# Kernel tuning notes

Measured on AMD Instinct MI355X. Metric: run time of the kernel, lower is better.

Reference implementation:

```python
import jax, jax.numpy as jnp
import numpy as np

NEG = -1000000000.0

def setup_inputs() -> dict:
    key = jax.random.key(0)
    k1, k2, k3, k4 = jax.random.split(key, 4)
    B, S, D = 8, 4096, 256
    query = jax.random.normal(k1, (B, S, D), dtype=jnp.float32)
    k_ = jax.random.normal(k2, (B, S, D), dtype=jnp.float32)
    value = jax.random.normal(k3, (B, S, D), dtype=jnp.float32)
    mask = jax.random.bernoulli(k4, 0.1, (B, S, 1))  # True = masked
    return {"query": query, "key": k_, "value": value, "mask": mask}

def reference(query, key, value, mask):
    # a: [B,S,1] sum of squares of query; b: [B,S,1] for key
    a = jnp.sum(query * query, axis=-1, keepdims=True)
    b = jnp.sum(key * key, axis=-1, keepdims=True)
    # s1 = (K^T / b) @ V  -> [B, D, D]; divide each key row s by b_s
    s1 = jnp.einsum('bsd,bse->bde', key / b, value)
    # score = Q / a, masked rows set to -1e9
    score = query / a
    score = jnp.where(mask, NEG, score)
    s2 = jnp.einsum('bsd,bde->bse', score, s1)
    return s2 / query.shape[-1]
```

## Files before the change

kernel.cpp:

```cpp
#include <hip/hip_runtime.h>

#define BB 8
#define SS 4096
#define DD 256
#define NEGV -1000000000.0f

typedef float f32x4 __attribute__((ext_vector_type(4)));
typedef short s16x8 __attribute__((ext_vector_type(8)));

static __device__ __forceinline__ unsigned short f2bf(float x) {
  unsigned int u = __builtin_bit_cast(unsigned int, x);
  u += 0x7fffu + ((u >> 16) & 1u);
  return (unsigned short)(u >> 16);
}

static __device__ __forceinline__ void gload_lds16(
    const unsigned short* __restrict__ g, unsigned short* l) {
  __builtin_amdgcn_global_load_lds(
      (const __attribute__((address_space(1))) void*)g,
      (__attribute__((address_space(3))) void*)l, 16, 0, 0);
}

__global__ __launch_bounds__(256) void prep_kernel(
    const float* __restrict__ Q, const float* __restrict__ K,
    const float* __restrict__ V, const int* __restrict__ mask,
    unsigned short* __restrict__ QS, unsigned short* __restrict__ KT,
    unsigned short* __restrict__ VT) {
  __shared__ unsigned short tile[64 * 260];
  const int b = blockIdx.y;
  const int s0 = blockIdx.x * 64;
  const int tid = threadIdx.x;
  const int w = tid >> 6, l = tid & 63;

  if (blockIdx.z == 0) {
    float4 reg[16];
    float ps[16];
#pragma unroll
    for (int it = 0; it < 16; ++it) {
      const int row = it * 4 + w;
      reg[it] = *(const float4*)(Q + ((size_t)b * SS + s0 + row) * DD + l * 4);
      ps[it] = reg[it].x * reg[it].x + reg[it].y * reg[it].y +
               reg[it].z * reg[it].z + reg[it].w * reg[it].w;
    }
#pragma unroll
    for (int off = 32; off; off >>= 1)
#pragma unroll
      for (int it = 0; it < 16; ++it) ps[it] += __shfl_xor(ps[it], off);
#pragma unroll
    for (int it = 0; it < 16; ++it) {
      const int row = it * 4 + w;
      const int m = mask[b * SS + s0 + row];
      const float ca = m ? 0.0f : (1.0f / ps[it]);
      const float aa = m ? NEGV : 0.0f;
      ushort4 o;
      o.x = f2bf(reg[it].x * ca + aa);
      o.y = f2bf(reg[it].y * ca + aa);
      o.z = f2bf(reg[it].z * ca + aa);
      o.w = f2bf(reg[it].w * ca + aa);
      *(ushort4*)(QS + ((size_t)b * SS + s0 + row) * DD + l * 4) = o;
    }
    return;
  }

  const int isK = (blockIdx.z == 1);
  const float* __restrict__ src = isK ? K : V;
  unsigned short* __restrict__ dst = isK ? KT : VT;

  float4 reg[16];
  float ps[16];
#pragma unroll
  for (int it = 0; it < 16; ++it) {
    const int row = it * 4 + w;
    reg[it] = *(const float4*)(src + ((size_t)b * SS + s0 + row) * DD + l * 4);
    ps[it] = reg[it].x * reg[it].x + reg[it].y * reg[it].y +
             reg[it].z * reg[it].z + reg[it].w * reg[it].w;
  }
  float scl[16];
  if (isK) {
#pragma unroll
    for (int off = 32; off; off >>= 1)
#pragma unroll
      for (int it = 0; it < 16; ++it) ps[it] += __shfl_xor(ps[it], off);
#pragma unroll
    for (int it = 0; it < 16; ++it) scl[it] = 1.0f / ps[it];
  } else {
#pragma unroll
    for (int it = 0; it < 16; ++it) scl[it] = 1.0f;
  }
#pragma unroll
  for (int it = 0; it < 16; ++it) {
    const int row = it * 4 + w;
    ushort4 o;
    o.x = f2bf(reg[it].x * scl[it]);
    o.y = f2bf(reg[it].y * scl[it]);
    o.z = f2bf(reg[it].z * scl[it]);
    o.w = f2bf(reg[it].w * scl[it]);
    *(ushort4*)(tile + row * 260 + l * 4) = o;
  }
  __syncthreads();
  const size_t gbase = ((size_t)b * DD + tid) * SS + s0;
#pragma unroll
  for (int c = 0; c < 8; ++c) {
    union { unsigned short h[8]; uint4 v; } u;
#pragma unroll
    for (int j = 0; j < 8; ++j) u.h[j] = tile[(c * 8 + j) * 260 + tid];
    *(uint4*)(dst + gbase + c * 8) = u.v;
  }
}

__global__ __launch_bounds__(256) void p2_kernel(
    const unsigned short* __restrict__ KT, const unsigned short* __restrict__ VT,
    float* __restrict__ part, int iters) {
  __shared__ unsigned short vt_l[128 * 64];
  __shared__ unsigned short kt_l[128 * 64];
  const int b = blockIdx.z;
  const int d0 = (blockIdx.x & 1) * 128;
  const int e0 = (blockIdx.x >> 1) * 128;
  const int sbeg = blockIdx.y * iters * 64;
  const int tid = threadIdx.x;
  const int w = tid >> 6, l = tid & 63;
  const int wr = w & 1, wc = w >> 1;
  const int quad = l >> 4, mr = l & 15;
  const int lr = l >> 3;
  const int lc = (l & 7) * 8;

  f32x4 acc[4][4];
#pragma unroll
  for (int i = 0; i < 4; ++i)
#pragma unroll
    for (int j = 0; j < 4; ++j) acc[i][j] = (f32x4){0.f, 0.f, 0.f, 0.f};

  const size_t vbase = ((size_t)b * DD + e0) * SS;
  const size_t kbase = ((size_t)b * DD + d0) * SS;

  for (int ks = 0; ks < iters; ++ks) {
    const int sc = sbeg + ks * 64;
#pragma unroll
    for (int c = 0; c < 4; ++c) {
      const int r0 = w * 32 + c * 8;
      gload_lds16(VT + vbase + (size_t)(r0 + lr) * SS + sc + lc, vt_l + r0 * 64);
      gload_lds16(KT + kbase + (size_t)(r0 + lr) * SS + sc + lc, kt_l + r0 * 64);
    }
    __syncthreads();
#pragma unroll
    for (int kh = 0; kh < 2; ++kh) {
      s16x8 af[4], bfr[4];
#pragma unroll
      for (int i = 0; i < 4; ++i)
        af[i] = *(const s16x8*)(vt_l + (wr * 64 + i * 16 + mr) * 64 + kh * 32 + quad * 8);
#pragma unroll
      for (int j = 0; j < 4; ++j)
        bfr[j] = *(const s16x8*)(kt_l + (wc * 64 + j * 16 + mr) * 64 + kh * 32 + quad * 8);
#pragma unroll
      for (int i = 0; i < 4; ++i)
#pragma unroll
        for (int j = 0; j < 4; ++j)
          acc[i][j] = __builtin_amdgcn_mfma_f32_16x16x32_bf16(af[i], bfr[j],
                                                              acc[i][j], 0, 0, 0);
    }
    __syncthreads();
  }

  float* pb = part + ((size_t)blockIdx.y * BB + b) * DD * DD;
#pragma unroll
  for (int i = 0; i < 4; ++i) {
    const int e = e0 + wr * 64 + i * 16 + quad * 4;
#pragma unroll
    for (int j = 0; j < 4; ++j) {
      const int d = d0 + wc * 64 + j * 16 + mr;
      float* p = pb + (size_t)e * DD + d;
#pragma unroll
      for (int r = 0; r < 4; ++r) p[(size_t)r * DD] = acc[i][j][r];
    }
  }
}

__global__ __launch_bounds__(256) void reduce_kernel(
    const float* __restrict__ part, unsigned short* __restrict__ s1b,
    int split) {
  const size_t i4 = ((size_t)blockIdx.x * 256 + threadIdx.x) * 4;
  float ax = 0.f, ay = 0.f, az = 0.f, aw = 0.f;
  for (int p = 0; p < split; ++p) {
    const float4 v = *(const float4*)(part + (size_t)p * (BB * DD * DD) + i4);
    ax += v.x; ay += v.y; az += v.z; aw += v.w;
  }
  ushort4 o;
  o.x = f2bf(ax); o.y = f2bf(ay); o.z = f2bf(az); o.w = f2bf(aw);
  *(ushort4*)(s1b + i4) = o;
}

__global__ __launch_bounds__(256) void p3_kernel(
    const unsigned short* __restrict__ QS, const unsigned short* __restrict__ s1b,
    float* __restrict__ out) {
  __shared__ unsigned short qs_l[128 * 64];
  __shared__ unsigned short s1_l[128 * 64];
  const int b = blockIdx.z;
  const int e0 = blockIdx.x * 128;
  const int s0 = blockIdx.y * 128;
  const int tid = threadIdx.x;
  const int w = tid >> 6, l = tid & 63;
  const int wr = w & 1, wc = w >> 1;
  const int quad = l >> 4, mr = l & 15;
  const int lr = l >> 3;
  const int lc = (l & 7) * 8;

  f32x4 acc[4][4];
#pragma unroll
  for (int i = 0; i < 4; ++i)
#pragma unroll
    for (int j = 0; j < 4; ++j) acc[i][j] = (f32x4){0.f, 0.f, 0.f, 0.f};

  for (int ks = 0; ks < 4; ++ks) {
    const int dc = ks * 64;
#pragma unroll
    for (int c = 0; c < 4; ++c) {
      const int r0 = w * 32 + c * 8;
      gload_lds16(QS + ((size_t)b * SS + s0 + r0 + lr) * DD + dc + lc,
                  qs_l + r0 * 64);
      gload_lds16(s1b + ((size_t)b * DD + e0 + r0 + lr) * DD + dc + lc,
                  s1_l + r0 * 64);
    }
    __syncthreads();
#pragma unroll
    for (int kh = 0; kh < 2; ++kh) {
      s16x8 af[4], bfr[4];
#pragma unroll
      for (int i = 0; i < 4; ++i)
        af[i] = *(const s16x8*)(qs_l + (wr * 64 + i * 16 + mr) * 64 + kh * 32 + quad * 8);
#pragma unroll
      for (int j = 0; j < 4; ++j)
        bfr[j] = *(const s16x8*)(s1_l + (wc * 64 + j * 16 + mr) * 64 + kh * 32 + quad * 8);
#pragma unroll
      for (int i = 0; i < 4; ++i)
#pragma unroll
        for (int j = 0; j < 4; ++j)
          acc[i][j] = __builtin_amdgcn_mfma_f32_16x16x32_bf16(af[i], bfr[j],
                                                              acc[i][j], 0, 0, 0);
    }
    __syncthreads();
  }

#pragma unroll
  for (int i = 0; i < 4; ++i) {
    const int s = s0 + wr * 64 + i * 16 + quad * 4;
#pragma unroll
    for (int j = 0; j < 4; ++j) {
      const int e = e0 + wc * 64 + j * 16 + mr;
      float* p = out + ((size_t)b * SS + s) * DD + e;
#pragma unroll
      for (int r = 0; r < 4; ++r) p[(size_t)r * DD] = acc[i][j][r] * (1.0f / DD);
    }
  }
}

extern "C" void kernel_launch(void* const* d_in, const int* in_sizes, int n_in,
                              void* d_out, int out_size, void* d_ws,
                              size_t ws_size, hipStream_t stream) {
  const float* Q = (const float*)d_in[0];
  const float* K = (const float*)d_in[1];
  const float* V = (const float*)d_in[2];
  const int* mask = (const int*)d_in[3];
  float* out = (float*)d_out;

  char* ws = (char*)d_ws;
  const size_t MB = (size_t)1024 * 1024;
  unsigned short* QS = (unsigned short*)(ws);
  unsigned short* KT = (unsigned short*)(ws + 16 * MB);
  unsigned short* VT = (unsigned short*)(ws + 32 * MB);
  float* part = (float*)(ws + 48 * MB);

  const int split = (ws_size >= (size_t)82 * MB) ? 16 : 8;
  const int iters = SS / (64 * split);
  unsigned short* s1b =
      (unsigned short*)(ws + 48 * MB + (size_t)split * 2 * MB);

  prep_kernel<<<dim3(SS / 64, BB, 3), 256, 0, stream>>>(Q, K, V, mask, QS, KT,
                                                        VT);
  p2_kernel<<<dim3(4, split, BB), 256, 0, stream>>>(KT, VT, part, iters);
  reduce_kernel<<<dim3(512), 256, 0, stream>>>(part, s1b, split);
  p3_kernel<<<dim3(2, SS / 128, BB), 256, 0, stream>>>(QS, s1b, out);
}
```

Before: 180.1 us.

## Split LDS tiles into K-halves to cut bank conflicts; hoist mask loads in prep

The p2 and p3 GEMM kernels now store each 64-wide K chunk in LDS as two 32-wide halves, so rows are 64 bytes apart instead of 128. This is meant to reduce LDS bank conflicts on the 16-byte MFMA fragment reads, while keeping the same global_load_lds loading pattern. In the prep kernel, all global loads, including the mask loads, are issued before any arithmetic so more memory requests are in flight, and a min-blocks hint of 2 is added to its launch bounds. The launch-bounds hint may limit register use and cause spills with 16 float4 values held per thread.

```diff
diff --git a/kernel.cpp b/kernel.cpp
--- a/kernel.cpp
+++ b/kernel.cpp
@@ -21,7 +21,7 @@
       (__attribute__((address_space(3))) void*)l, 16, 0, 0);
 }
 
-__global__ __launch_bounds__(256) void prep_kernel(
+__global__ __launch_bounds__(256, 2) void prep_kernel(
     const float* __restrict__ Q, const float* __restrict__ K,
     const float* __restrict__ V, const int* __restrict__ mask,
     unsigned short* __restrict__ QS, unsigned short* __restrict__ KT,
@@ -39,9 +39,14 @@
     for (int it = 0; it < 16; ++it) {
       const int row = it * 4 + w;
       reg[it] = *(const float4*)(Q + ((size_t)b * SS + s0 + row) * DD + l * 4);
+    }
+    int mk[16];
+#pragma unroll
+    for (int it = 0; it < 16; ++it) mk[it] = mask[b * SS + s0 + it * 4 + w];
+#pragma unroll
+    for (int it = 0; it < 16; ++it)
       ps[it] = reg[it].x * reg[it].x + reg[it].y * reg[it].y +
                reg[it].z * reg[it].z + reg[it].w * reg[it].w;
-    }
 #pragma unroll
     for (int off = 32; off; off >>= 1)
 #pragma unroll
@@ -49,9 +54,8 @@
 #pragma unroll
     for (int it = 0; it < 16; ++it) {
       const int row = it * 4 + w;
-      const int m = mask[b * SS + s0 + row];
-      const float ca = m ? 0.0f : (1.0f / ps[it]);
-      const float aa = m ? NEGV : 0.0f;
+      const float ca = mk[it] ? 0.0f : (1.0f / ps[it]);
+      const float aa = mk[it] ? NEGV : 0.0f;
       ushort4 o;
       o.x = f2bf(reg[it].x * ca + aa);
       o.y = f2bf(reg[it].y * ca + aa);
@@ -72,9 +76,11 @@
   for (int it = 0; it < 16; ++it) {
     const int row = it * 4 + w;
     reg[it] = *(const float4*)(src + ((size_t)b * SS + s0 + row) * DD + l * 4);
+  }
+#pragma unroll
+  for (int it = 0; it < 16; ++it)
     ps[it] = reg[it].x * reg[it].x + reg[it].y * reg[it].y +
              reg[it].z * reg[it].z + reg[it].w * reg[it].w;
-  }
   float scl[16];
   if (isK) {
 #pragma unroll
@@ -111,8 +117,8 @@
 __global__ __launch_bounds__(256) void p2_kernel(
     const unsigned short* __restrict__ KT, const unsigned short* __restrict__ VT,
     float* __restrict__ part, int iters) {
-  __shared__ unsigned short vt_l[128 * 64];
-  __shared__ unsigned short kt_l[128 * 64];
+  __shared__ unsigned short vt_l[2][128 * 32];
+  __shared__ unsigned short kt_l[2][128 * 32];
   const int b = blockIdx.z;
   const int d0 = (blockIdx.x & 1) * 128;
   const int e0 = (blockIdx.x >> 1) * 128;
@@ -121,8 +127,8 @@
   const int w = tid >> 6, l = tid & 63;
   const int wr = w & 1, wc = w >> 1;
   const int quad = l >> 4, mr = l & 15;
-  const int lr = l >> 3;
-  const int lc = (l & 7) * 8;
+  const int lr = l >> 2;
+  const int lc = (l & 3) * 8;
 
   f32x4 acc[4][4];
 #pragma unroll
@@ -136,21 +142,25 @@
   for (int ks = 0; ks < iters; ++ks) {
     const int sc = sbeg + ks * 64;
 #pragma unroll
-    for (int c = 0; c < 4; ++c) {
-      const int r0 = w * 32 + c * 8;
-      gload_lds16(VT + vbase + (size_t)(r0 + lr) * SS + sc + lc, vt_l + r0 * 64);
-      gload_lds16(KT + kbase + (size_t)(r0 + lr) * SS + sc + lc, kt_l + r0 * 64);
-    }
+    for (int h = 0; h < 2; ++h)
+#pragma unroll
+      for (int g = 0; g < 2; ++g) {
+        const int r0 = w * 32 + g * 16;
+        gload_lds16(VT + vbase + (size_t)(r0 + lr) * SS + sc + h * 32 + lc,
+                    &vt_l[h][r0 * 32]);
+        gload_lds16(KT + kbase + (size_t)(r0 + lr) * SS + sc + h * 32 + lc,
+                    &kt_l[h][r0 * 32]);
+      }
     __syncthreads();
 #pragma unroll
     for (int kh = 0; kh < 2; ++kh) {
       s16x8 af[4], bfr[4];
 #pragma unroll
       for (int i = 0; i < 4; ++i)
-        af[i] = *(const s16x8*)(vt_l + (wr * 64 + i * 16 + mr) * 64 + kh * 32 + quad * 8);
+        af[i] = *(const s16x8*)(&vt_l[kh][(wr * 64 + i * 16 + mr) * 32 + quad * 8]);
 #pragma unroll
       for (int j = 0; j < 4; ++j)
-        bfr[j] = *(const s16x8*)(kt_l + (wc * 64 + j * 16 + mr) * 64 + kh * 32 + quad * 8);
+        bfr[j] = *(const s16x8*)(&kt_l[kh][(wc * 64 + j * 16 + mr) * 32 + quad * 8]);
 #pragma unroll
       for (int i = 0; i < 4; ++i)
 #pragma unroll
@@ -192,8 +202,8 @@
 __global__ __launch_bounds__(256) void p3_kernel(
     const unsigned short* __restrict__ QS, const unsigned short* __restrict__ s1b,
     float* __restrict__ out) {
-  __shared__ unsigned short qs_l[128 * 64];
-  __shared__ unsigned short s1_l[128 * 64];
+  __shared__ unsigned short qs_l[2][128 * 32];
+  __shared__ unsigned short s1_l[2][128 * 32];
   const int b = blockIdx.z;
   const int e0 = blockIdx.x * 128;
   const int s0 = blockIdx.y * 128;
@@ -201,8 +211,8 @@
   const int w = tid >> 6, l = tid & 63;
   const int wr = w & 1, wc = w >> 1;
   const int quad = l >> 4, mr = l & 15;
-  const int lr = l >> 3;
-  const int lc = (l & 7) * 8;
+  const int lr = l >> 2;
+  const int lc = (l & 3) * 8;
 
   f32x4 acc[4][4];
 #pragma unroll
@@ -213,23 +223,25 @@
   for (int ks = 0; ks < 4; ++ks) {
     const int dc = ks * 64;
 #pragma unroll
-    for (int c = 0; c < 4; ++c) {
-      const int r0 = w * 32 + c * 8;
-      gload_lds16(QS + ((size_t)b * SS + s0 + r0 + lr) * DD + dc + lc,
-                  qs_l + r0 * 64);
-      gload_lds16(s1b + ((size_t)b * DD + e0 + r0 + lr) * DD + dc + lc,
-                  s1_l + r0 * 64);
-    }
+    for (int h = 0; h < 2; ++h)
+#pragma unroll
+      for (int g = 0; g < 2; ++g) {
+        const int r0 = w * 32 + g * 16;
+        gload_lds16(QS + ((size_t)b * SS + s0 + r0 + lr) * DD + dc + h * 32 + lc,
+                    &qs_l[h][r0 * 32]);
+        gload_lds16(s1b + ((size_t)b * DD + e0 + r0 + lr) * DD + dc + h * 32 + lc,
+                    &s1_l[h][r0 * 32]);
+      }
     __syncthreads();
 #pragma unroll
     for (int kh = 0; kh < 2; ++kh) {
       s16x8 af[4], bfr[4];
 #pragma unroll
       for (int i = 0; i < 4; ++i)
-        af[i] = *(const s16x8*)(qs_l + (wr * 64 + i * 16 + mr) * 64 + kh * 32 + quad * 8);
+        af[i] = *(const s16x8*)(&qs_l[kh][(wr * 64 + i * 16 + mr) * 32 + quad * 8]);
 #pragma unroll
       for (int j = 0; j < 4; ++j)
-        bfr[j] = *(const s16x8*)(s1_l + (wc * 64 + j * 16 + mr) * 64 + kh * 32 + quad * 8);
+        bfr[j] = *(const s16x8*)(&s1_l[kh][(wc * 64 + j * 16 + mr) * 32 + quad * 8]);
 #pragma unroll
       for (int i = 0; i < 4; ++i)
 #pragma unroll
```

New measurement: 178.0 us. No clear change (-1.1%).
